# Kernel tuning notes

Hardware: AMD Instinct MI355X
Metric: run time of the kernel (lower is better)

Reference implementation:

```python
import jax, jax.numpy as jnp
import numpy as np

B, O, OBS, A, H = 512, 16, 128, 4, 64 * 8  # H=512
H = 512
LN_EPS = 1e-5


def _lin_init(key, fan_in, fan_out):
    k1, k2 = jax.random.split(key)
    lim = 1.0 / np.sqrt(fan_in)
    W = jax.random.uniform(k1, (fan_in, fan_out), jnp.float32, -lim, lim)
    b = jax.random.uniform(k2, (fan_out,), jnp.float32, -lim, lim)
    return W, b


def setup_inputs() -> dict:
    key = jax.random.key(0)
    ks = jax.random.split(key, 10)
    states = jax.random.normal(ks[0], (B, O, OBS), jnp.float32)
    action = jax.random.randint(ks[1], (B,), 0, A * O, jnp.int64)
    eW1, eb1 = _lin_init(ks[2], 2 * OBS, H)
    eW2, eb2 = _lin_init(ks[3], H, H)
    eW3, eb3 = _lin_init(ks[4], H, H)
    nW1, nb1 = _lin_init(ks[5], H + OBS + A, H)
    nW2, nb2 = _lin_init(ks[6], H, H)
    nW3, nb3 = _lin_init(ks[7], H, OBS)
    return dict(states=states, action=action,
                eW1=eW1, eb1=eb1, eW2=eW2, eb2=eb2,
                eg=jnp.ones((H,), jnp.float32), ebeta=jnp.zeros((H,), jnp.float32),
                eW3=eW3, eb3=eb3,
                nW1=nW1, nb1=nb1, nW2=nW2, nb2=nb2,
                ng=jnp.ones((H,), jnp.float32), nbeta=jnp.zeros((H,), jnp.float32),
                nW3=nW3, nb3=nb3)


def _ln(x, g, b):
    mu = jnp.mean(x, axis=-1, keepdims=True)
    var = jnp.mean((x - mu) ** 2, axis=-1, keepdims=True)
    return (x - mu) * jax.lax.rsqrt(var + LN_EPS) * g + b


def _mlp(x, W1, b1, W2, b2, g, beta, W3, b3):
    h = jax.nn.relu(x @ W1 + b1)
    h = jax.nn.relu(_ln(h @ W2 + b2, g, beta))
    return h @ W3 + b3


def _edge_index():
    # torch nonzero order: (i, j) for i in range(O), j != i; then batch offsets
    i = jnp.arange(O)[:, None]                   # [O,1]
    k = jnp.arange(O - 1)[None, :]               # [1,O-1]
    j = k + (k >= i)                             # skip self-loop
    row_l = jnp.broadcast_to(i, (O, O - 1)).reshape(-1)
    col_l = j.reshape(-1)
    off = (jnp.arange(B) * O)[:, None]           # [B,1]
    row = (row_l[None, :] + off).reshape(-1)     # [B*O*(O-1)]
    col = (col_l[None, :] + off).reshape(-1)
    return row, col


def reference(states, action, eW1, eb1, eW2, eb2, eg, ebeta, eW3, eb3,
              nW1, nb1, nW2, nb2, ng, nbeta, nW3, nb3):
    nodes = states.reshape(B * O, OBS)
    row, col = _edge_index()
    # edge model: gather pairs -> MLP
    e_in = jnp.concatenate([nodes[row], nodes[col]], axis=1)    # [E, 2*OBS]
    edge_attr = _mlp(e_in, eW1, eb1, eW2, eb2, eg, ebeta, eW3, eb3)  # [E, H]
    # action: one-hot over A*O, reshaped per-node
    act_vec = jax.nn.one_hot(action, A * O, dtype=states.dtype).reshape(B * O, A)
    node_in = jnp.concatenate([nodes, act_vec], axis=1)         # [B*O, OBS+A]
    # scatter: unsorted segment sum over source index (row)
    agg = jax.ops.segment_sum(edge_attr, row, num_segments=B * O)  # [B*O, H]
    node_in = jnp.concatenate([node_in, agg], axis=1)           # [B*O, OBS+A+H]
    out = _mlp(node_in, nW1, nb1, nW2, nb2, ng, nbeta, nW3, nb3)
    return out.reshape(B, O, OBS)
```

## Files before the change

kernel.cpp:

```cpp
#include <hip/hip_runtime.h>
#include <hip/hip_bf16.h>


using bf16 = __hip_bfloat16;
typedef __attribute__((ext_vector_type(8))) short bf16x8;
typedef __attribute__((ext_vector_type(4))) short short4v;
typedef __attribute__((ext_vector_type(4))) float f32x4;

#define LDK 40
#define LDQ 1032
#define LDN 520
#define LDT 72

__device__ __forceinline__ short f2bf(float f) {
  bf16 h = __float2bfloat16(f);
  return *reinterpret_cast<short*>(&h);
}
__device__ __forceinline__ float bs2f(short s) {
  bf16 h = *reinterpret_cast<bf16*>(&s);
  return __bfloat162float(h);
}
__device__ __forceinline__ f32x4 mfma16(bf16x8 a, bf16x8 b, f32x4 c) {
  return __builtin_amdgcn_mfma_f32_16x16x32_bf16(a, b, c, 0, 0, 0);
}
__device__ __forceinline__ bf16x8 ld8f(const float* p) {
  float4 a = *(const float4*)p;
  float4 b = *(const float4*)(p + 4);
  bf16x8 o;
  o[0] = f2bf(a.x); o[1] = f2bf(a.y); o[2] = f2bf(a.z); o[3] = f2bf(a.w);
  o[4] = f2bf(b.x); o[5] = f2bf(b.y); o[6] = f2bf(b.z); o[7] = f2bf(b.w);
  return o;
}

__global__ __launch_bounds__(256) void mega_prep(
    const float* __restrict__ eW3, short* __restrict__ eW3b,
    const float* __restrict__ nW1, unsigned short* __restrict__ nW1at,
    const float* __restrict__ eW1, short* __restrict__ eW1f,
    const float* __restrict__ eW2, short* __restrict__ eW2f,
    short* __restrict__ nW1nf, const float* __restrict__ nW2,
    short* __restrict__ nW2f, const float* __restrict__ nW3,
    short* __restrict__ nW3f) {
  __shared__ unsigned short ttile[32][33];
  __shared__ short ftile[32 * LDT];
  const int z = blockIdx.z, bx = blockIdx.x, t = threadIdx.x;
  if (z == 0) {
    if (bx >= 256) return;
    int i = (bx * 256 + t) * 4;
    float4 v = *(const float4*)(eW3 + i);
    short4v o;
    o.x = f2bf(v.x); o.y = f2bf(v.y); o.z = f2bf(v.z); o.w = f2bf(v.w);
    *(short4v*)(eW3b + i) = o;
    return;
  }
  if (z == 1) {
    if (bx >= 256) return;
    const float* src = nW1 + 132 * 512;
    int bc = (bx & 15) * 32, br = (bx >> 4) * 32;
    int tx = t & 31, ty = t >> 5;
    for (int i = ty; i < 32; i += 8) {
      short s = f2bf(src[(size_t)(br + i) * 512 + bc + tx]);
      ttile[i][tx] = *reinterpret_cast<unsigned short*>(&s);
    }
    __syncthreads();
    for (int i = ty; i < 32; i += 8)
      nW1at[(size_t)(bc + i) * 512 + br + tx] = ttile[tx][i];
    return;
  }
  const float* W;
  short* out;
  int ldw, kts, gq, goff, tot_sh;
  switch (z) {
    case 2: W = eW1;           out = eW1f;  ldw = 512; kts = 4;  gq = 8; goff = 0;  tot_sh = 6; break;
    case 3: W = eW1 + 128*512; out = eW1f;  ldw = 512; kts = 4;  gq = 8; goff = 32; tot_sh = 6; break;
    case 4: W = eW2;           out = eW2f;  ldw = 512; kts = 16; gq = 8; goff = 0;  tot_sh = 5; break;
    case 5: W = nW1;           out = nW1nf; ldw = 512; kts = 4;  gq = 8; goff = 0;  tot_sh = 5; break;
    case 6: W = nW2;           out = nW2f;  ldw = 512; kts = 16; gq = 8; goff = 0;  tot_sh = 5; break;
    default: W = nW3;          out = nW3f;  ldw = 128; kts = 16; gq = 2; goff = 0;  tot_sh = 3; break;
  }
  if (bx >= kts * gq) return;
  const int kt = bx / gq, qg = bx % gq;
  {
    int r = t >> 3, c0 = (t & 7) * 8;
    const float* src = W + (size_t)(kt * 32 + r) * ldw + qg * 64 + c0;
    *(bf16x8*)&ftile[r * LDT + c0] = ld8f(src);
  }
  __syncthreads();
  {
    int og = t >> 6, lane = t & 63, q = lane >> 4, lc = lane & 15;
    int gg = qg * 4 + og;
    size_t base = ((size_t)((kt << tot_sh) + gg + goff)) << 9;
    bf16x8 v;
#pragma unroll
    for (int j = 0; j < 8; ++j) v[j] = ftile[(q * 8 + j) * LDT + og * 16 + lc];
    *(bf16x8*)(out + base + lane * 8) = v;
  }
}

__global__ __launch_bounds__(256) void combo96(
    const bf16* __restrict__ nW1at, const bf16* __restrict__ eW3b,
    short* __restrict__ Wcf, const float* __restrict__ eb3,
    const float* __restrict__ nb1, const float* __restrict__ nW1,
    float* __restrict__ bfold) {
  __shared__ short Al[64 * LDK];
  __shared__ short Bl[64 * LDK];
  __shared__ float red[256];
  const int bid = blockIdx.x;
  const int t = threadIdx.x;
  const int wid = t >> 6, lane = t & 63, q = lane >> 4, lc = lane & 15;
  const f32x4 zz = {0.f, 0.f, 0.f, 0.f};

  if (bid < 64) {
    const int wm = wid >> 1, wn = wid & 1;
    const int n0 = (bid >> 3) * 64, k0 = (bid & 7) * 64;
    f32x4 acc[2][2];
#pragma unroll
    for (int mb = 0; mb < 2; ++mb)
#pragma unroll
      for (int nb = 0; nb < 2; ++nb) acc[mb][nb] = zz;
    const int sr = t >> 2, seg = t & 3;
    for (int h0 = 0; h0 < 512; h0 += 32) {
      *(uint4*)&Al[sr * LDK + seg * 8] =
          *(const uint4*)(nW1at + (size_t)(n0 + sr) * 512 + h0 + seg * 8);
      *(uint4*)&Bl[sr * LDK + seg * 8] =
          *(const uint4*)(eW3b + (size_t)(k0 + sr) * 512 + h0 + seg * 8);
      __syncthreads();
      bf16x8 af[2], bfr[2];
#pragma unroll
      for (int mb = 0; mb < 2; ++mb)
        af[mb] = *(const bf16x8*)&Al[(wm * 32 + mb * 16 + lc) * LDK + q * 8];
#pragma unroll
      for (int nb = 0; nb < 2; ++nb)
        bfr[nb] = *(const bf16x8*)&Bl[(wn * 32 + nb * 16 + lc) * LDK + q * 8];
#pragma unroll
      for (int mb = 0; mb < 2; ++mb)
#pragma unroll
        for (int nb = 0; nb < 2; ++nb)
          acc[mb][nb] = mfma16(af[mb], bfr[nb], acc[mb][nb]);
      __syncthreads();
    }
#pragma unroll
    for (int mb = 0; mb < 2; ++mb)
#pragma unroll
      for (int nb = 0; nb < 2; ++nb)
#pragma unroll
        for (int r = 0; r < 4; ++r) {
          int n = n0 + wm * 32 + mb * 16 + q * 4 + r;
          int k = k0 + wn * 32 + nb * 16 + lc;
          int kt = k >> 5, kin = k & 31, qf = kin >> 3, jf = kin & 7;
          Wcf[(((size_t)kt * 32 + (n >> 4)) * 64 + qf * 16 + (n & 15)) * 8 +
              jf] = f2bf(acc[mb][nb][r]);
        }
    return;
  }
  {
    const int n = (bid - 64) * 16 + (t & 15);
    const int sl = t >> 4;
    float s = 0.f;
#pragma unroll 8
    for (int h = sl * 32; h < sl * 32 + 32; ++h)
      s += eb3[h] * nW1[(size_t)(132 + h) * 512 + n];
    red[sl * 16 + (t & 15)] = s;
    __syncthreads();
    if (t < 16) {
      float tot = 0.f;
#pragma unroll
      for (int k = 0; k < 16; ++k) tot += red[k * 16 + t];
      bfold[(bid - 64) * 16 + t] = nb1[(bid - 64) * 16 + t] + 15.f * tot;
    }
  }
}

__global__ __launch_bounds__(512, 4) void mega(
    const float* __restrict__ states, const int* __restrict__ action,
    const bf16* __restrict__ eW1f, const float* __restrict__ eb1,
    const bf16* __restrict__ eW2f, const float* __restrict__ eb2,
    const float* __restrict__ eg, const float* __restrict__ ebt,
    const bf16* __restrict__ nW1nf, const bf16* __restrict__ Wcf,
    const bf16* __restrict__ nW2f, const bf16* __restrict__ nW3f,
    const float* __restrict__ bfold, const float* __restrict__ nW1,
    const float* __restrict__ nb2, const float* __restrict__ ng,
    const float* __restrict__ nbt, const float* __restrict__ nb3,
    float* __restrict__ Out) {
  __shared__ __align__(16) char smem[64000];
  short* PQL = (short*)(smem);
  short* sts = (short*)(smem + 33024);
  short* Ab = (short*)(smem + 33024);
  float* s_sum = (float*)(smem + 43264);
  float* s_sq = (float*)(smem + 45312);
  short* SL = (short*)(smem + 47360);
  short* n1s = PQL;

  const int t = threadIdx.x;
  const int w = t >> 6, lane = t & 63, q = lane >> 4, lc = lane & 15;
  const int bb = blockIdx.x;
  const f32x4 zz = {0.f, 0.f, 0.f, 0.f};

  if (t < 256) {
    int r = t >> 4, c8 = (t & 15) * 8;
    *(bf16x8*)&sts[r * 136 + c8] =
        ld8f(states + ((size_t)bb * 16 + r) * 128 + c8);
  }
  __syncthreads();

  {
    f32x4 acc[8];
#pragma unroll
    for (int nb = 0; nb < 8; ++nb) acc[nb] = zz;
#pragma unroll
    for (int kt = 0; kt < 4; ++kt) {
      bf16x8 af = *(const bf16x8*)&sts[lc * 136 + kt * 32 + q * 8];
#pragma unroll
      for (int nb = 0; nb < 8; ++nb) {
        bf16x8 bfr = *(const bf16x8*)(eW1f +
                                      (((size_t)kt * 64 + w * 8 + nb) * 64 +
                                       lane) * 8);
        acc[nb] = mfma16(af, bfr, acc[nb]);
      }
    }
#pragma unroll
    for (int nb = 0; nb < 8; ++nb) {
      int col = w * 128 + nb * 16 + lc;
      float bv = (col < 512) ? eb1[col] : 0.f;
#pragma unroll
      for (int r = 0; r < 4; ++r)
        PQL[(q * 4 + r) * LDQ + col] = f2bf(acc[nb][r] + bv);
    }
  }
  __syncthreads();

  const int ar = t >> 3;
  const int kk = (t & 7) * 4;
  const int gA = ar >> 4;
  const int slot = ar & 15;
  const bool padA = (slot == 15);
#pragma unroll 1
  for (int sg = 0; sg < 4; ++sg) {
    const int srcb = sg * 4 + gA;
    const int dstb = padA ? 0 : slot + (slot >= srcb ? 1 : 0);
    const short* pA = PQL + srcb * LDQ + kk;
    const short* qA = PQL + dstb * LDQ + 512 + kk;

    f32x4 acc[4][4];
#pragma unroll
    for (int mb = 0; mb < 4; ++mb)
#pragma unroll
      for (int nb = 0; nb < 4; ++nb) acc[mb][nb] = zz;

    auto buildA = [&](int kt, int buf) {
      short4v av = {0, 0, 0, 0};
      if (!padA) {
        short4v pv = *(const short4v*)(pA + kt * 32);
        short4v qv = *(const short4v*)(qA + kt * 32);
        av.x = f2bf(fmaxf(bs2f(pv.x) + bs2f(qv.x), 0.f));
        av.y = f2bf(fmaxf(bs2f(pv.y) + bs2f(qv.y), 0.f));
        av.z = f2bf(fmaxf(bs2f(pv.z) + bs2f(qv.z), 0.f));
        av.w = f2bf(fmaxf(bs2f(pv.w) + bs2f(qv.w), 0.f));
      }
      *(short4v*)&Ab[buf * 2560 + ar * LDK + kk] = av;
    };

    buildA(0, 0);
#pragma unroll 1
    for (int kt = 0; kt < 16; ++kt) {
      __syncthreads();
      const int cur = kt & 1;
      bf16x8 bfr[4], af[4];
#pragma unroll
      for (int nb = 0; nb < 4; ++nb)
        bfr[nb] = *(const bf16x8*)(eW2f +
                                   (((size_t)kt * 32 + w * 4 + nb) * 64 + lane) *
                                       8);
#pragma unroll
      for (int mb = 0; mb < 4; ++mb)
        af[mb] = *(const bf16x8*)&Ab[cur * 2560 + (mb * 16 + lc) * LDK + q * 8];
      if (kt < 15) buildA(kt + 1, cur ^ 1);
#pragma unroll
      for (int mb = 0; mb < 4; ++mb)
#pragma unroll
        for (int nb = 0; nb < 4; ++nb)
          acc[mb][nb] = mfma16(af[mb], bfr[nb], acc[mb][nb]);
    }

    float bv[4], gv[4], bev[4];
#pragma unroll
    for (int nb = 0; nb < 4; ++nb) {
      int col = w * 64 + nb * 16 + lc;
      bv[nb] = eb2[col];
      gv[nb] = eg[col];
      bev[nb] = ebt[col];
    }
#pragma unroll
    for (int mb = 0; mb < 4; ++mb)
#pragma unroll
      for (int nb = 0; nb < 4; ++nb)
#pragma unroll
        for (int r = 0; r < 4; ++r) acc[mb][nb][r] += bv[nb];

#pragma unroll
    for (int mb = 0; mb < 4; ++mb) {
      float ps[4] = {0, 0, 0, 0}, pq2[4] = {0, 0, 0, 0};
#pragma unroll
      for (int nb = 0; nb < 4; ++nb)
#pragma unroll
        for (int r = 0; r < 4; ++r) {
          float x = acc[mb][nb][r];
          ps[r] += x;
          pq2[r] += x * x;
        }
#pragma unroll
      for (int d = 1; d < 16; d <<= 1)
#pragma unroll
        for (int r = 0; r < 4; ++r) {
          ps[r] += __shfl_xor(ps[r], d, 64);
          pq2[r] += __shfl_xor(pq2[r], d, 64);
        }
      if (lc == 0)
#pragma unroll
        for (int r = 0; r < 4; ++r) {
          int row = mb * 16 + q * 4 + r;
          s_sum[row * 8 + w] = ps[r];
          s_sq[row * 8 + w] = pq2[r];
        }
    }
    __syncthreads();
#pragma unroll
    for (int mb = 0; mb < 4; ++mb) {
      float sv[4] = {0, 0, 0, 0};
#pragma unroll
      for (int r = 0; r < 4; ++r) {
        int row = mb * 16 + q * 4 + r;
        float tot = 0.f, tsq = 0.f;
#pragma unroll
        for (int wv = 0; wv < 8; ++wv) {
          tot += s_sum[row * 8 + wv];
          tsq += s_sq[row * 8 + wv];
        }
        float m = tot * (1.f / 512.f);
        float rstd = rsqrtf(tsq * (1.f / 512.f) - m * m + 1e-5f);
#pragma unroll
        for (int nb = 0; nb < 4; ++nb) {
          float h = (acc[mb][nb][r] - m) * rstd * gv[nb] + bev[nb];
          h = fmaxf(h, 0.f);
          if (q * 4 + r != 15) sv[nb] += h;
        }
      }
#pragma unroll
      for (int nb = 0; nb < 4; ++nb) {
        sv[nb] += __shfl_xor(sv[nb], 16, 64);
        sv[nb] += __shfl_xor(sv[nb], 32, 64);
      }
      if (lane < 16)
#pragma unroll
        for (int nb = 0; nb < 4; ++nb)
          SL[(sg * 4 + mb) * LDN + w * 64 + nb * 16 + lc] = f2bf(sv[nb]);
    }
    __syncthreads();
  }

  if (t < 256) {
    int r = t >> 4, c8 = (t & 15) * 8;
    *(bf16x8*)&sts[r * 136 + c8] =
        ld8f(states + ((size_t)bb * 16 + r) * 128 + c8);
  }
  __syncthreads();

  {
    f32x4 acc[4];
#pragma unroll
    for (int nb = 0; nb < 4; ++nb) acc[nb] = zz;
#pragma unroll
    for (int kt = 0; kt < 4; ++kt) {
      bf16x8 af = *(const bf16x8*)&sts[lc * 136 + kt * 32 + q * 8];
#pragma unroll
      for (int nb = 0; nb < 4; ++nb) {
        bf16x8 bfr = *(const bf16x8*)(nW1nf +
                                      (((size_t)kt * 32 + w * 4 + nb) * 64 +
                                       lane) * 8);
        acc[nb] = mfma16(af, bfr, acc[nb]);
      }
    }
#pragma unroll 2
    for (int kt = 0; kt < 16; ++kt) {
      bf16x8 af = *(const bf16x8*)&SL[lc * LDN + kt * 32 + q * 8];
#pragma unroll
      for (int nb = 0; nb < 4; ++nb) {
        bf16x8 bfr = *(const bf16x8*)(Wcf +
                                      (((size_t)kt * 32 + w * 4 + nb) * 64 +
                                       lane) * 8);
        acc[nb] = mfma16(af, bfr, acc[nb]);
      }
    }
    int a = action[bb];
    int aw = a >> 2, ac4 = a & 3;
#pragma unroll
    for (int nb = 0; nb < 4; ++nb) {
      int col = w * 64 + nb * 16 + lc;
      float bv = bfold[col];
      float awv = nW1[(size_t)(128 + ac4) * 512 + col];
#pragma unroll
      for (int r = 0; r < 4; ++r) {
        int row = q * 4 + r;
        float x = acc[nb][r] + bv + (row == aw ? awv : 0.f);
        n1s[row * LDN + col] = f2bf(fmaxf(x, 0.f));
      }
    }
  }
  __syncthreads();

  {
    f32x4 acc[4];
#pragma unroll
    for (int nb = 0; nb < 4; ++nb) acc[nb] = zz;
#pragma unroll 2
    for (int kt = 0; kt < 16; ++kt) {
      bf16x8 af = *(const bf16x8*)&n1s[lc * LDN + kt * 32 + q * 8];
#pragma unroll
      for (int nb = 0; nb < 4; ++nb) {
        bf16x8 bfr = *(const bf16x8*)(nW2f +
                                      (((size_t)kt * 32 + w * 4 + nb) * 64 +
                                       lane) * 8);
        acc[nb] = mfma16(af, bfr, acc[nb]);
      }
    }
    float gv[4], bev[4];
    float ps[4] = {0, 0, 0, 0}, pq2[4] = {0, 0, 0, 0};
#pragma unroll
    for (int nb = 0; nb < 4; ++nb) {
      int col = w * 64 + nb * 16 + lc;
      float bv = nb2[col];
      gv[nb] = ng[col];
      bev[nb] = nbt[col];
#pragma unroll
      for (int r = 0; r < 4; ++r) {
        acc[nb][r] += bv;
        ps[r] += acc[nb][r];
        pq2[r] += acc[nb][r] * acc[nb][r];
      }
    }
#pragma unroll
    for (int d = 1; d < 16; d <<= 1)
#pragma unroll
      for (int r = 0; r < 4; ++r) {
        ps[r] += __shfl_xor(ps[r], d, 64);
        pq2[r] += __shfl_xor(pq2[r], d, 64);
      }
    if (lc == 0)
#pragma unroll
      for (int r = 0; r < 4; ++r) {
        s_sum[(q * 4 + r) * 8 + w] = ps[r];
        s_sq[(q * 4 + r) * 8 + w] = pq2[r];
      }
    __syncthreads();
#pragma unroll
    for (int r = 0; r < 4; ++r) {
      int row = q * 4 + r;
      float tot = 0.f, tsq = 0.f;
#pragma unroll
      for (int wv = 0; wv < 8; ++wv) {
        tot += s_sum[row * 8 + wv];
        tsq += s_sq[row * 8 + wv];
      }
      float m = tot * (1.f / 512.f);
      float rstd = rsqrtf(tsq * (1.f / 512.f) - m * m + 1e-5f);
#pragma unroll
      for (int nb = 0; nb < 4; ++nb) {
        int col = w * 64 + nb * 16 + lc;
        float h = (acc[nb][r] - m) * rstd * gv[nb] + bev[nb];
        n1s[row * LDN + col] = f2bf(fmaxf(h, 0.f));
      }
    }
  }
  __syncthreads();

  {
    f32x4 acc3 = zz;
#pragma unroll 2
    for (int kt = 0; kt < 16; ++kt) {
      bf16x8 af = *(const bf16x8*)&n1s[lc * LDN + kt * 32 + q * 8];
      bf16x8 bfr = *(const bf16x8*)(nW3f +
                                    (((size_t)kt * 8 + w) * 64 + lane) * 8);
      acc3 = mfma16(af, bfr, acc3);
    }
    int col = w * 16 + lc;
    float b3 = nb3[col];
#pragma unroll
    for (int r = 0; r < 4; ++r)
      Out[((size_t)bb * 16 + q * 4 + r) * 128 + col] = acc3[r] + b3;
  }
}

extern "C" void kernel_launch(void* const* d_in, const int* in_sizes, int n_in,
                              void* d_out, int out_size, void* d_ws,
                              size_t ws_size, hipStream_t stream) {
  const float* states = (const float*)d_in[0];
  const int* action = (const int*)d_in[1];
  const float* eW1 = (const float*)d_in[2];
  const float* eb1 = (const float*)d_in[3];
  const float* eW2 = (const float*)d_in[4];
  const float* eb2 = (const float*)d_in[5];
  const float* eg = (const float*)d_in[6];
  const float* ebt = (const float*)d_in[7];
  const float* eW3 = (const float*)d_in[8];
  const float* eb3 = (const float*)d_in[9];
  const float* nW1 = (const float*)d_in[10];
  const float* nb1 = (const float*)d_in[11];
  const float* nW2 = (const float*)d_in[12];
  const float* nb2 = (const float*)d_in[13];
  const float* ng = (const float*)d_in[14];
  const float* nbt = (const float*)d_in[15];
  const float* nW3 = (const float*)d_in[16];
  const float* nb3 = (const float*)d_in[17];

  char* w = (char*)d_ws;
  bf16* eW1f = (bf16*)w;     w += (size_t)131072 * 2;
  bf16* eW2f = (bf16*)w;     w += (size_t)262144 * 2;
  bf16* nW1nf = (bf16*)w;    w += (size_t)65536 * 2;
  bf16* nW2f = (bf16*)w;     w += (size_t)262144 * 2;
  bf16* nW3f = (bf16*)w;     w += (size_t)65536 * 2;
  bf16* Wcf = (bf16*)w;      w += (size_t)262144 * 2;
  bf16* eW3b = (bf16*)w;     w += (size_t)262144 * 2;
  bf16* nW1at = (bf16*)w;    w += (size_t)262144 * 2;
  float* bfold = (float*)w;  w += (size_t)512 * 4;

  mega_prep<<<dim3(256, 1, 8), 256, 0, stream>>>(
      eW3, (short*)eW3b, nW1, (unsigned short*)nW1at, eW1, (short*)eW1f, eW2,
      (short*)eW2f, (short*)nW1nf, nW2, (short*)nW2f, nW3, (short*)nW3f);

  combo96<<<96, 256, 0, stream>>>(nW1at, eW3b, (short*)Wcf, eb3, nb1, nW1,
                                  bfold);

  mega<<<512, 512, 0, stream>>>(states, action, eW1f, eb1, eW2f, eb2, eg, ebt,
                                nW1nf, Wcf, nW2f, nW3f, bfold, nW1, nb2, ng,
                                nbt, nb3, (float*)d_out);

  (void)in_sizes; (void)n_in; (void)out_size; (void)ws_size;
}
```

Before: 245.5 us.

## Triple-buffer swizzled edge A tiles with K=64 steps and precomputed LN stats

The edge layer-2 GEMM loop now builds 64-wide K slices of the ReLU(P+Q) operand into a triple-buffered, XOR-swizzled LDS tile. This halves the number of barriers per slice and removes bank conflicts. MFMA bursts are bracketed with s_setprio, and barriers use an explicit lgkmcnt wait. LayerNorm mean and rstd are now computed once per row by a few threads into shared memory instead of redundantly by every lane, with padded stat arrays. The larger LDS footprint (about 79 KB) may lower the number of resident blocks per CU.

```diff
diff --git a/kernel.cpp b/kernel.cpp
--- a/kernel.cpp
+++ b/kernel.cpp
@@ -30,6 +30,11 @@
   o[0] = f2bf(a.x); o[1] = f2bf(a.y); o[2] = f2bf(a.z); o[3] = f2bf(a.w);
   o[4] = f2bf(b.x); o[5] = f2bf(b.y); o[6] = f2bf(b.z); o[7] = f2bf(b.w);
   return o;
+}
+__device__ __forceinline__ void lgkm0_barrier() {
+  asm volatile("s_waitcnt lgkmcnt(0)" ::: "memory");
+  __builtin_amdgcn_s_barrier();
+  asm volatile("" ::: "memory");
 }
 
 __global__ __launch_bounds__(256) void mega_prep(
@@ -181,13 +186,14 @@
     const float* __restrict__ nb2, const float* __restrict__ ng,
     const float* __restrict__ nbt, const float* __restrict__ nb3,
     float* __restrict__ Out) {
-  __shared__ __align__(16) char smem[64000];
+  __shared__ __align__(16) char smem[79360];
   short* PQL = (short*)(smem);
   short* sts = (short*)(smem + 33024);
-  short* Ab = (short*)(smem + 33024);
-  float* s_sum = (float*)(smem + 43264);
-  float* s_sq = (float*)(smem + 45312);
-  short* SL = (short*)(smem + 47360);
+  short* AbS = (short*)(smem + 33024);
+  float* s_sum = (float*)(smem + 57600);
+  float* s_sq = (float*)(smem + 59904);
+  float* mr = (float*)(smem + 62208);
+  short* SL = (short*)(smem + 62720);
   short* n1s = PQL;
 
   const int t = threadIdx.x;
@@ -229,16 +235,31 @@
   __syncthreads();
 
   const int ar = t >> 3;
-  const int kk = (t & 7) * 4;
+  const int j8 = t & 7;
   const int gA = ar >> 4;
   const int slot = ar & 15;
   const bool padA = (slot == 15);
+  const int wu = j8 ^ (ar & 7);
+
 #pragma unroll 1
   for (int sg = 0; sg < 4; ++sg) {
     const int srcb = sg * 4 + gA;
     const int dstb = padA ? 0 : slot + (slot >= srcb ? 1 : 0);
-    const short* pA = PQL + srcb * LDQ + kk;
-    const short* qA = PQL + dstb * LDQ + 512 + kk;
+    const short* pA = PQL + srcb * LDQ + j8 * 8;
+    const short* qA = PQL + dstb * LDQ + 512 + j8 * 8;
+    short* const wdst0 = AbS + ar * 64 + wu * 8;
+
+    auto build = [&](int ks, int buf) {
+      bf16x8 av = {0, 0, 0, 0, 0, 0, 0, 0};
+      if (!padA) {
+        bf16x8 pv = *(const bf16x8*)(pA + ks * 64);
+        bf16x8 qv = *(const bf16x8*)(qA + ks * 64);
+#pragma unroll
+        for (int e = 0; e < 8; ++e)
+          av[e] = f2bf(fmaxf(bs2f(pv[e]) + bs2f(qv[e]), 0.f));
+      }
+      *(bf16x8*)(wdst0 + buf * 4096) = av;
+    };
 
     f32x4 acc[4][4];
 #pragma unroll
@@ -246,39 +267,52 @@
 #pragma unroll
       for (int nb = 0; nb < 4; ++nb) acc[mb][nb] = zz;
 
-    auto buildA = [&](int kt, int buf) {
-      short4v av = {0, 0, 0, 0};
-      if (!padA) {
-        short4v pv = *(const short4v*)(pA + kt * 32);
-        short4v qv = *(const short4v*)(qA + kt * 32);
-        av.x = f2bf(fmaxf(bs2f(pv.x) + bs2f(qv.x), 0.f));
-        av.y = f2bf(fmaxf(bs2f(pv.y) + bs2f(qv.y), 0.f));
-        av.z = f2bf(fmaxf(bs2f(pv.z) + bs2f(qv.z), 0.f));
-        av.w = f2bf(fmaxf(bs2f(pv.w) + bs2f(qv.w), 0.f));
-      }
-      *(short4v*)&Ab[buf * 2560 + ar * LDK + kk] = av;
-    };
-
-    buildA(0, 0);
+    build(0, 0);
+    lgkm0_barrier();
+
+    int cur = 0, nxt = 1;
 #pragma unroll 1
-    for (int kt = 0; kt < 16; ++kt) {
-      __syncthreads();
-      const int cur = kt & 1;
-      bf16x8 bfr[4], af[4];
+    for (int ks = 0; ks < 8; ++ks) {
+      const short* Abc = AbS + cur * 4096;
+      bf16x8 a0[4], b0[4];
+#pragma unroll
+      for (int mb = 0; mb < 4; ++mb)
+        a0[mb] =
+            *(const bf16x8*)&Abc[(mb * 16 + lc) * 64 + ((q ^ (lc & 7)) * 8)];
 #pragma unroll
       for (int nb = 0; nb < 4; ++nb)
-        bfr[nb] = *(const bf16x8*)(eW2f +
-                                   (((size_t)kt * 32 + w * 4 + nb) * 64 + lane) *
-                                       8);
+        b0[nb] = *(const bf16x8*)(eW2f +
+                                  (((size_t)(ks * 2) * 32 + w * 4 + nb) * 64 +
+                                   lane) * 8);
+      if (ks < 7) build(ks + 1, nxt);
+      lgkm0_barrier();
+      __builtin_amdgcn_s_setprio(1);
 #pragma unroll
       for (int mb = 0; mb < 4; ++mb)
-        af[mb] = *(const bf16x8*)&Ab[cur * 2560 + (mb * 16 + lc) * LDK + q * 8];
-      if (kt < 15) buildA(kt + 1, cur ^ 1);
+#pragma unroll
+        for (int nb = 0; nb < 4; ++nb)
+          acc[mb][nb] = mfma16(a0[mb], b0[nb], acc[mb][nb]);
+      __builtin_amdgcn_s_setprio(0);
+      bf16x8 a1[4], b1[4];
+#pragma unroll
+      for (int nb = 0; nb < 4; ++nb)
+        b1[nb] = *(const bf16x8*)(eW2f +
+                                  (((size_t)(ks * 2 + 1) * 32 + w * 4 + nb) *
+                                       64 + lane) * 8);
 #pragma unroll
       for (int mb = 0; mb < 4; ++mb)
+        a1[mb] = *(const bf16x8*)&Abc[(mb * 16 + lc) * 64 +
+                                      (((4 + q) ^ (lc & 7)) * 8)];
+      __builtin_amdgcn_s_setprio(1);
+#pragma unroll
+      for (int mb = 0; mb < 4; ++mb)
 #pragma unroll
         for (int nb = 0; nb < 4; ++nb)
-          acc[mb][nb] = mfma16(af[mb], bfr[nb], acc[mb][nb]);
+          acc[mb][nb] = mfma16(a1[mb], b1[nb], acc[mb][nb]);
+      __builtin_amdgcn_s_setprio(0);
+      cur = nxt;
+      nxt = nxt + 1;
+      if (nxt == 3) nxt = 0;
     }
 
     float bv[4], gv[4], bev[4];
@@ -290,20 +324,14 @@
       bev[nb] = ebt[col];
     }
 #pragma unroll
-    for (int mb = 0; mb < 4; ++mb)
-#pragma unroll
-      for (int nb = 0; nb < 4; ++nb)
-#pragma unroll
-        for (int r = 0; r < 4; ++r) acc[mb][nb][r] += bv[nb];
-
-#pragma unroll
     for (int mb = 0; mb < 4; ++mb) {
       float ps[4] = {0, 0, 0, 0}, pq2[4] = {0, 0, 0, 0};
 #pragma unroll
       for (int nb = 0; nb < 4; ++nb)
 #pragma unroll
         for (int r = 0; r < 4; ++r) {
-          float x = acc[mb][nb][r];
+          float x = acc[mb][nb][r] + bv[nb];
+          acc[mb][nb][r] = x;
           ps[r] += x;
           pq2[r] += x * x;
         }
@@ -318,9 +346,21 @@
 #pragma unroll
         for (int r = 0; r < 4; ++r) {
           int row = mb * 16 + q * 4 + r;
-          s_sum[row * 8 + w] = ps[r];
-          s_sq[row * 8 + w] = pq2[r];
+          s_sum[row * 9 + w] = ps[r];
+          s_sq[row * 9 + w] = pq2[r];
         }
+    }
+    __syncthreads();
+    if (t < 64) {
+      float tot = 0.f, tsq = 0.f;
+#pragma unroll
+      for (int wv = 0; wv < 8; ++wv) {
+        tot += s_sum[t * 9 + wv];
+        tsq += s_sq[t * 9 + wv];
+      }
+      float m = tot * (1.f / 512.f);
+      mr[t * 2] = m;
+      mr[t * 2 + 1] = rsqrtf(tsq * (1.f / 512.f) - m * m + 1e-5f);
     }
     __syncthreads();
 #pragma unroll
@@ -329,14 +369,7 @@
 #pragma unroll
       for (int r = 0; r < 4; ++r) {
         int row = mb * 16 + q * 4 + r;
-        float tot = 0.f, tsq = 0.f;
-#pragma unroll
-        for (int wv = 0; wv < 8; ++wv) {
-          tot += s_sum[row * 8 + wv];
-          tsq += s_sq[row * 8 + wv];
-        }
-        float m = tot * (1.f / 512.f);
-        float rstd = rsqrtf(tsq * (1.f / 512.f) - m * m + 1e-5f);
+        float m = mr[row * 2], rstd = mr[row * 2 + 1];
 #pragma unroll
         for (int nb = 0; nb < 4; ++nb) {
           float h = (acc[mb][nb][r] - m) * rstd * gv[nb] + bev[nb];
@@ -354,8 +387,8 @@
         for (int nb = 0; nb < 4; ++nb)
           SL[(sg * 4 + mb) * LDN + w * 64 + nb * 16 + lc] = f2bf(sv[nb]);
     }
-    __syncthreads();
-  }
+  }
+  __syncthreads();
 
   if (t < 256) {
     int r = t >> 4, c8 = (t & 15) * 8;
@@ -447,21 +480,26 @@
     if (lc == 0)
 #pragma unroll
       for (int r = 0; r < 4; ++r) {
-        s_sum[(q * 4 + r) * 8 + w] = ps[r];
-        s_sq[(q * 4 + r) * 8 + w] = pq2[r];
-      }
+        s_sum[(q * 4 + r) * 9 + w] = ps[r];
+        s_sq[(q * 4 + r) * 9 + w] = pq2[r];
+      }
+    __syncthreads();
+    if (t < 16) {
+      float tot = 0.f, tsq = 0.f;
+#pragma unroll
+      for (int wv = 0; wv < 8; ++wv) {
+        tot += s_sum[t * 9 + wv];
+        tsq += s_sq[t * 9 + wv];
+      }
+      float m = tot * (1.f / 512.f);
+      mr[t * 2] = m;
+      mr[t * 2 + 1] = rsqrtf(tsq * (1.f / 512.f) - m * m + 1e-5f);
+    }
     __syncthreads();
 #pragma unroll
     for (int r = 0; r < 4; ++r) {
       int row = q * 4 + r;
-      float tot = 0.f, tsq = 0.f;
-#pragma unroll
-      for (int wv = 0; wv < 8; ++wv) {
-        tot += s_sum[row * 8 + wv];
-        tsq += s_sq[row * 8 + wv];
-      }
-      float m = tot * (1.f / 512.f);
-      float rstd = rsqrtf(tsq * (1.f / 512.f) - m * m + 1e-5f);
+      float m = mr[row * 2], rstd = mr[row * 2 + 1];
 #pragma unroll
       for (int nb = 0; nb < 4; ++nb) {
         int col = w * 64 + nb * 16 + lc;
```

Result: no change. 248.8 us (+1.4%).
